# Kernel optimization log

Hardware: AMD Instinct MI355X
Metric: run time of the kernel (lower is better)

The kernel has to match this reference:

```python
import jax, jax.numpy as jnp
import numpy as np

B, N, F, D, H = 4, 2048, 128, 64, 4
NEG = -1000000000.0


def setup_inputs() -> dict:
    key = jax.random.key(0)
    k1, k2, k3, k4 = jax.random.split(key, 4)
    X = jax.random.normal(k1, (B, N, F), dtype=jnp.float32)
    A = jax.random.randint(k2, (N, N), 0, 2, dtype=jnp.int32)
    kernels = jax.random.normal(k3, (H, F, D), dtype=jnp.float32) * 0.1
    attn_kernels = jax.random.normal(k4, (H, D), dtype=jnp.float32) * 0.1
    return {"X": X, "A": A, "kernels": kernels, "attn_kernels": attn_kernels}


def reference(X, A, kernels, attn_kernels):
    # h: per-head linear projection  [H,B,N,D]
    h = jnp.einsum('bnf,hfd->hbnd', X, kernels)
    # per-node scalar scores e_i = h @ a  [H,B,N]
    s = jnp.einsum('hbnd,hd->hbn', h, attn_kernels)
    # pairwise additive score e_ij = relu(s_i + s_j)  [H,B,N,N]
    e = jax.nn.relu(s[:, :, :, None] + s[:, :, None, :])
    e = jnp.where(A[None, None, :, :] > 0, e, NEG)
    alpha = jax.nn.softmax(e, axis=-1)
    # dropout is identity at inference
    h_prime = jnp.einsum('hbnm,hbmd->hbnd', alpha, h)
    out = jnp.mean(h_prime, axis=0)           # mean over heads -> [B,N,D]
    return jax.nn.leaky_relu(out, negative_slope=0.2)
```

## Files before the change

### kernel.cpp

```cpp
#include <hip/hip_runtime.h>
#include <hip/hip_bf16.h>
#include <hip/hip_fp16.h>

typedef __attribute__((ext_vector_type(8))) short short8;
typedef __attribute__((ext_vector_type(8))) _Float16 f16x8;
typedef __attribute__((ext_vector_type(2))) _Float16 f16x2;
typedef __attribute__((ext_vector_type(4))) float f32x4;
typedef __attribute__((ext_vector_type(4))) unsigned int u32x4;
typedef unsigned short u16;
typedef unsigned int u32;

constexpr int CB = 4, CN = 2048, CF = 128, CD = 64, CH = 4;
constexpr int IT = 32;

__device__ inline u32 fmap(float f) {
    u32 b = __float_as_uint(f);
    return b ^ ((u32)(((int)b) >> 31) | 0x80000000u);
}
__device__ inline float funmap(u32 u) {
    u32 b = (u & 0x80000000u) ? (u ^ 0x80000000u) : ~u;
    return __uint_as_float(b);
}
__device__ inline u16 bf16bits(float v) {
    __hip_bfloat16 b = __float2bfloat16(v);
    return *reinterpret_cast<u16*>(&b);
}

__global__ __launch_bounds__(256) void prep_k(const int* __restrict__ A,
                                              const float* __restrict__ W,
                                              u32* __restrict__ mask,
                                              u32* __restrict__ smax_u,
                                              u16* __restrict__ WThi,
                                              u16* __restrict__ WTlo) {
    int blk = blockIdx.x, t = threadIdx.x;
    if (blk < 16384) {
        int gid = blk * 256 + t;
        if (blk == 0 && t < CH * CB) smax_u[t] = 0u;
        unsigned long long mk = __ballot(A[gid] > 0);
        if ((t & 63) == 0) {
            mask[gid >> 5] = (u32)mk;
            mask[(gid >> 5) + 1] = (u32)(mk >> 32);
        }
    } else {
        int idx = (blk - 16384) * 256 + t;
        int e = idx & 7;
        int l = (idx >> 3) & 63;
        int dt = (idx >> 9) & 3;
        int kk = (idx >> 11) & 3;
        int h = idx >> 13;
        int f = kk * 32 + (l >> 4) * 8 + e;
        int d = dt * 16 + (l & 15);
        float v = W[(h * CF + f) * CD + d];
        __hip_bfloat16 bh = __float2bfloat16(v);
        WThi[idx] = *reinterpret_cast<u16*>(&bh);
        WTlo[idx] = bf16bits(v - __bfloat162float(bh));
    }
}

__global__ __launch_bounds__(256, 2) void proj_k(const float* __restrict__ X,
                                                 const u16* __restrict__ WThi,
                                                 const u16* __restrict__ WTlo,
                                                 const float* __restrict__ AK,
                                                 u16* __restrict__ hT,
                                                 float* __restrict__ sout,
                                                 u16* __restrict__ eout,
                                                 u32* __restrict__ smax_u) {
    __shared__ float tr[4][CD][17];

    int blk = blockIdx.x;
    int ntile = blk & 127;
    int b = blk >> 7;
    int n0 = ntile * 16;
    int t = threadIdx.x;
    int w = t >> 6, l = t & 63;
    int h = w;
    int row_l = l & 15, jg = l >> 4;

    const float* xrow = X + ((size_t)b * CN + n0 + row_l) * CF + jg * 8;
    const short8* whiU = reinterpret_cast<const short8*>(WThi) + (size_t)h * 1024 + l;
    const short8* wloU = reinterpret_cast<const short8*>(WTlo) + (size_t)h * 1024 + l;

    float4 xa[4], xb[4];
#pragma unroll
    for (int kk = 0; kk < 4; ++kk) {
        xa[kk] = *reinterpret_cast<const float4*>(xrow + kk * 32);
        xb[kk] = *reinterpret_cast<const float4*>(xrow + kk * 32 + 4);
    }
    short8 bhi[4][4], blo[4][4];
#pragma unroll
    for (int kk = 0; kk < 4; ++kk)
#pragma unroll
        for (int dt = 0; dt < 4; ++dt) {
            bhi[kk][dt] = whiU[(kk * 4 + dt) * 64];
            blo[kk][dt] = wloU[(kk * 4 + dt) * 64];
        }

    f32x4 c[4];
    f32x4 zero = {0.f, 0.f, 0.f, 0.f};
#pragma unroll
    for (int dt = 0; dt < 4; ++dt) c[dt] = zero;

#pragma unroll
    for (int kk = 0; kk < 4; ++kk) {
        float xv[8] = {xa[kk].x, xa[kk].y, xa[kk].z, xa[kk].w,
                       xb[kk].x, xb[kk].y, xb[kk].z, xb[kk].w};
        short8 ahi, alo;
#pragma unroll
        for (int e = 0; e < 8; ++e) {
            __hip_bfloat16 bh = __float2bfloat16(xv[e]);
            ahi[e] = (short)*reinterpret_cast<u16*>(&bh);
            alo[e] = (short)bf16bits(xv[e] - __bfloat162float(bh));
        }
#pragma unroll
        for (int dt = 0; dt < 4; ++dt) {
            c[dt] = __builtin_amdgcn_mfma_f32_16x16x32_bf16(ahi, bhi[kk][dt], c[dt], 0, 0, 0);
            c[dt] = __builtin_amdgcn_mfma_f32_16x16x32_bf16(ahi, blo[kk][dt], c[dt], 0, 0, 0);
            c[dt] = __builtin_amdgcn_mfma_f32_16x16x32_bf16(alo, bhi[kk][dt], c[dt], 0, 0, 0);
        }
    }

    float av[4];
#pragma unroll
    for (int dt = 0; dt < 4; ++dt) av[dt] = AK[h * CD + dt * 16 + row_l];
    float sacc[4];
#pragma unroll
    for (int r = 0; r < 4; ++r)
        sacc[r] = c[0][r] * av[0] + c[1][r] * av[1] + c[2][r] * av[2] + c[3][r] * av[3];
#pragma unroll
    for (int off = 1; off <= 8; off <<= 1)
#pragma unroll
        for (int r = 0; r < 4; ++r) sacc[r] += __shfl_xor(sacc[r], off, 64);

    float mx = fmaxf(fmaxf(sacc[0], sacc[1]), fmaxf(sacc[2], sacc[3]));
    mx = fmaxf(mx, __shfl_xor(mx, 16, 64));
    mx = fmaxf(mx, __shfl_xor(mx, 32, 64));
    if (l == 0) atomicMax(&smax_u[h * CB + b], fmap(mx));

    if (row_l == 0) {
#pragma unroll
        for (int r = 0; r < 4; ++r) {
            size_t si = (size_t)(h * CB + b) * CN + n0 + jg * 4 + r;
            sout[si] = sacc[r];
            _Float16 ev = (_Float16)__expf(sacc[r]);
            eout[si] = *reinterpret_cast<u16*>(&ev);
        }
    }

#pragma unroll
    for (int dt = 0; dt < 4; ++dt)
#pragma unroll
        for (int r = 0; r < 4; ++r) tr[w][dt * 16 + row_l][jg * 4 + r] = c[dt][r];
    __syncthreads();

    f16x8* hTs = reinterpret_cast<f16x8*>(hT);
    int jc = l >> 5, d0 = l & 31;
#pragma unroll
    for (int half = 0; half < 2; ++half) {
        f16x8 pk;
#pragma unroll
        for (int e = 0; e < 8; ++e)
            pk[e] = (_Float16)tr[w][half * 32 + d0][jc * 8 + e];
        hTs[((size_t)(h * CB + b) * 256 + ntile * 2 + jc) * 64 + half * 32 + d0] = pk;
    }
}

__global__ __launch_bounds__(1024, 4) void attn_k(const u16* __restrict__ hT,
                                                  const float* __restrict__ s_ws,
                                                  const u32* __restrict__ e_ws32,
                                                  const u32* __restrict__ smax_u,
                                                  const u32* __restrict__ mask32,
                                                  float* __restrict__ out) {
    __shared__ u32 e_sl[CH][CN / 2];
    __shared__ u32 m_lds[IT][65];
    __shared__ float cbuf[CH][2][IT][68];
    __shared__ float lbuf[CH][4][IT];

    int orig = blockIdx.x;
    int xcd = orig & 7, pos = orig >> 3;
    int b = xcd >> 1;
    int it = (xcd & 1) * 32 + pos;
    int i0 = it * IT;
    int t = threadIdx.x, w = t >> 6, l = t & 63;
    int hq = w >> 2, jq = w & 3;
    int row_l = l & 15, jg = l >> 4;

    for (int idx = t; idx < CH * (CN / 2); idx += 1024) {
        int hh = idx >> 10, j = idx & 1023;
        e_sl[hh][j] = e_ws32[(size_t)(hh * CB + b) * (CN / 2) + j];
    }
    for (int idx = t; idx < IT * 64; idx += 1024) {
        int r = idx >> 6, wd = idx & 63;
        m_lds[r][wd] = mask32[(size_t)(i0 + r) * 64 + wd];
    }
    __syncthreads();

    float smax = funmap(smax_u[hq * CB + b]);
    float si0 = s_ws[(size_t)(hq * CB + b) * CN + i0 + row_l];
    float si1 = s_ws[(size_t)(hq * CB + b) * CN + i0 + 16 + row_l];
    float m0 = fmaxf(si0 + smax, 0.f), m1 = fmaxf(si1 + smax, 0.f);
    _Float16 ei0s = (_Float16)__expf(si0 - m0), ci0s = (_Float16)__expf(-m0);
    _Float16 ei1s = (_Float16)__expf(si1 - m1), ci1s = (_Float16)__expf(-m1);
    f16x2 Ei0 = {ei0s, ei0s}, Ci0 = {ci0s, ci0s};
    f16x2 Ei1 = {ei1s, ei1s}, Ci1 = {ci1s, ci1s};

    f32x4 c0[4], c1[4], cl0, cl1;
    f32x4 zero = {0.f, 0.f, 0.f, 0.f};
#pragma unroll
    for (int dt = 0; dt < 4; ++dt) { c0[dt] = zero; c1[dt] = zero; }
    cl0 = zero; cl1 = zero;

    f16x8 ones;
#pragma unroll
    for (int e = 0; e < 8; ++e) ones[e] = (_Float16)1.0f;

    const f16x8* hp = reinterpret_cast<const f16x8*>(hT) +
                      ((size_t)(hq * CB + b) * 256 + jq * 64 + jg) * 64 + row_l;

    f16x8 bfA[4], bfB[4];
#pragma unroll
    for (int dt = 0; dt < 4; ++dt) bfA[dt] = hp[dt * 16];

#define ATTN_STEP(KK, BCUR, BNXT, KNXT)                                          \
    do {                                                                         \
        _Pragma("unroll") for (int dt = 0; dt < 4; ++dt)                         \
            BNXT[dt] = hp[(KNXT) * 256 + dt * 16];                               \
        int jw = jq * 256 + (KK) * 16 + jg * 4;                                  \
        u32x4 ejw = *reinterpret_cast<const u32x4*>(&e_sl[hq][jw]);              \
        u32 by0 = m_lds[row_l][jq * 16 + (KK)] >> (jg * 8);                      \
        u32 by1 = m_lds[16 + row_l][jq * 16 + (KK)] >> (jg * 8);                 \
        u32x4 af0w, af1w;                                                        \
        _Pragma("unroll") for (int p = 0; p < 4; ++p) {                          \
            u32 ewv = ejw[p];                                                    \
            f16x2 e2 = __builtin_bit_cast(f16x2, ewv);                           \
            f16x2 t0 = __builtin_elementwise_max(Ei0 * e2, Ci0);                 \
            f16x2 t1 = __builtin_elementwise_max(Ei1 * e2, Ci1);                 \
            u32 mk0 = (((by0 >> (2 * p)) & 1u) ? 0xFFFFu : 0u) |                 \
                      (((by0 >> (2 * p + 1)) & 1u) ? 0xFFFF0000u : 0u);          \
            u32 mk1 = (((by1 >> (2 * p)) & 1u) ? 0xFFFFu : 0u) |                 \
                      (((by1 >> (2 * p + 1)) & 1u) ? 0xFFFF0000u : 0u);          \
            af0w[p] = __builtin_bit_cast(u32, t0) & mk0;                         \
            af1w[p] = __builtin_bit_cast(u32, t1) & mk1;                         \
        }                                                                        \
        f16x8 af0 = __builtin_bit_cast(f16x8, af0w);                             \
        f16x8 af1 = __builtin_bit_cast(f16x8, af1w);                             \
        __builtin_amdgcn_s_setprio(1);                                           \
        _Pragma("unroll") for (int dt = 0; dt < 4; ++dt) {                       \
            c0[dt] = __builtin_amdgcn_mfma_f32_16x16x32_f16(af0, BCUR[dt], c0[dt], 0, 0, 0); \
            c1[dt] = __builtin_amdgcn_mfma_f32_16x16x32_f16(af1, BCUR[dt], c1[dt], 0, 0, 0); \
        }                                                                        \
        cl0 = __builtin_amdgcn_mfma_f32_16x16x32_f16(af0, ones, cl0, 0, 0, 0);   \
        cl1 = __builtin_amdgcn_mfma_f32_16x16x32_f16(af1, ones, cl1, 0, 0, 0);   \
        __builtin_amdgcn_s_setprio(0);                                           \
    } while (0)

#pragma unroll 1
    for (int kp = 0; kp < 16; kp += 2) {
        ATTN_STEP(kp, bfA, bfB, kp + 1);
        int kn = (kp + 2 < 16) ? kp + 2 : 15;
        ATTN_STEP(kp + 1, bfB, bfA, kn);
    }
#undef ATTN_STEP

    int slot = jq & 1;
    if (row_l == 0)
#pragma unroll
        for (int r = 0; r < 4; ++r) {
            lbuf[hq][jq][jg * 4 + r] = cl0[r];
            lbuf[hq][jq][16 + jg * 4 + r] = cl1[r];
        }
    if (jq < 2) {
#pragma unroll
        for (int dt = 0; dt < 4; ++dt)
#pragma unroll
            for (int r = 0; r < 4; ++r) {
                cbuf[hq][slot][jg * 4 + r][dt * 16 + row_l] = c0[dt][r];
                cbuf[hq][slot][16 + jg * 4 + r][dt * 16 + row_l] = c1[dt][r];
            }
    }
    __syncthreads();
    if (jq >= 2) {
#pragma unroll
        for (int dt = 0; dt < 4; ++dt)
#pragma unroll
            for (int r = 0; r < 4; ++r) {
                cbuf[hq][slot][jg * 4 + r][dt * 16 + row_l] += c0[dt][r];
                cbuf[hq][slot][16 + jg * 4 + r][dt * 16 + row_l] += c1[dt][r];
            }
    }
    __syncthreads();

    for (int idx = t; idx < IT * CD; idx += 1024) {
        int row = idx >> 6, d = idx & 63;
        float acc = 0.f;
#pragma unroll
        for (int h = 0; h < CH; ++h) {
            float num = cbuf[h][0][row][d] + cbuf[h][1][row][d];
            float den = lbuf[h][0][row] + lbuf[h][1][row] + lbuf[h][2][row] + lbuf[h][3][row];
            acc += num / fmaxf(den, 1e-30f);
        }
        float o = acc * 0.25f;
        out[((size_t)b * CN + i0 + row) * CD + d] = o > 0.f ? o : 0.2f * o;
    }
}

extern "C" void kernel_launch(void* const* d_in, const int* in_sizes, int n_in,
                              void* d_out, int out_size, void* d_ws, size_t ws_size,
                              hipStream_t stream) {
    const float* X  = (const float*)d_in[0];
    const int*   A  = (const int*)d_in[1];
    const float* W  = (const float*)d_in[2];
    const float* AK = (const float*)d_in[3];
    float* out = (float*)d_out;

    char* wp = (char*)d_ws;
    float* s_ws = (float*)wp;    wp += 131072;
    u16* e_ws = (u16*)wp;        wp += 131072;
    u32* smax_ws = (u32*)wp;     wp += 256;
    u32* mask_ws = (u32*)wp;     wp += 524288;
    u16* hT = (u16*)wp;          wp += 4194304;
    u16* WThi = (u16*)wp;        wp += 65536;
    u16* WTlo = (u16*)wp;        wp += 65536;

    prep_k<<<16384 + 128, 256, 0, stream>>>(A, W, mask_ws, smax_ws, WThi, WTlo);
    proj_k<<<CB * (CN / 16), 256, 0, stream>>>(X, WThi, WTlo, AK, hT, s_ws, e_ws, smax_ws);
    attn_k<<<CB * (CN / IT), 1024, 0, stream>>>(hT, s_ws, (const u32*)e_ws,
                                                smax_ws, mask_ws, out);
}
```

Before: 59.40 us.

## Fuse adjacency-mask build and weight split into projection kernel

Removes the separate prep kernel. The projection kernel now builds the adjacency bitmask itself, using the h==0 blocks, and splits weights into bf16 hi/lo on the fly from a shared-memory copy of W. The projection grid is reorganised so each block handles one head and 64 rows, and smax is zeroed with a memset instead. This saves a kernel launch and the WThi/WTlo round-trip through global memory. The cost is extra per-MFMA conversion work, 32KB of LDS per block, and load imbalance, since only a quarter of the blocks do the mask work.

```diff
diff --git a/kernel.cpp b/kernel.cpp
--- a/kernel.cpp
+++ b/kernel.cpp
@@ -26,74 +26,49 @@
     return *reinterpret_cast<u16*>(&b);
 }
 
-__global__ __launch_bounds__(256) void prep_k(const int* __restrict__ A,
-                                              const float* __restrict__ W,
-                                              u32* __restrict__ mask,
-                                              u32* __restrict__ smax_u,
-                                              u16* __restrict__ WThi,
-                                              u16* __restrict__ WTlo) {
-    int blk = blockIdx.x, t = threadIdx.x;
-    if (blk < 16384) {
-        int gid = blk * 256 + t;
-        if (blk == 0 && t < CH * CB) smax_u[t] = 0u;
-        unsigned long long mk = __ballot(A[gid] > 0);
-        if ((t & 63) == 0) {
-            mask[gid >> 5] = (u32)mk;
-            mask[(gid >> 5) + 1] = (u32)(mk >> 32);
-        }
-    } else {
-        int idx = (blk - 16384) * 256 + t;
-        int e = idx & 7;
-        int l = (idx >> 3) & 63;
-        int dt = (idx >> 9) & 3;
-        int kk = (idx >> 11) & 3;
-        int h = idx >> 13;
-        int f = kk * 32 + (l >> 4) * 8 + e;
-        int d = dt * 16 + (l & 15);
-        float v = W[(h * CF + f) * CD + d];
-        __hip_bfloat16 bh = __float2bfloat16(v);
-        WThi[idx] = *reinterpret_cast<u16*>(&bh);
-        WTlo[idx] = bf16bits(v - __bfloat162float(bh));
-    }
-}
-
-__global__ __launch_bounds__(256, 2) void proj_k(const float* __restrict__ X,
-                                                 const u16* __restrict__ WThi,
-                                                 const u16* __restrict__ WTlo,
+__global__ __launch_bounds__(256, 4) void proj_k(const float* __restrict__ X,
+                                                 const int* __restrict__ A,
+                                                 const float* __restrict__ W,
                                                  const float* __restrict__ AK,
                                                  u16* __restrict__ hT,
                                                  float* __restrict__ sout,
                                                  u16* __restrict__ eout,
-                                                 u32* __restrict__ smax_u) {
+                                                 u32* __restrict__ smax_u,
+                                                 u32* __restrict__ mask_ws) {
+    __shared__ float wbuf[CF * CD];
     __shared__ float tr[4][CD][17];
 
     int blk = blockIdx.x;
-    int ntile = blk & 127;
     int b = blk >> 7;
-    int n0 = ntile * 16;
-    int t = threadIdx.x;
-    int w = t >> 6, l = t & 63;
-    int h = w;
+    int h = (blk >> 5) & 3;
+    int tile4 = blk & 31;
+    int t = threadIdx.x, w = t >> 6, l = t & 63;
     int row_l = l & 15, jg = l >> 4;
+    int n0 = tile4 * 64 + w * 16;
+
+    if (h == 0) {
+        int rowbase = tile4 * 64 + b * 16;
+        for (int iter = 0; iter < 128; ++iter) {
+            int idx = iter * 256 + t;
+            int rl2 = idx >> 11, col = idx & 2047;
+            unsigned long long mk = __ballot(A[(size_t)(rowbase + rl2) * CN + col] > 0);
+            if (l == 0) {
+                mask_ws[(rowbase + rl2) * 64 + (col >> 5)] = (u32)mk;
+                mask_ws[(rowbase + rl2) * 64 + (col >> 5) + 1] = (u32)(mk >> 32);
+            }
+        }
+    }
+
+    for (int idx = t; idx < CF * CD; idx += 256) wbuf[idx] = W[(size_t)h * CF * CD + idx];
+    __syncthreads();
 
     const float* xrow = X + ((size_t)b * CN + n0 + row_l) * CF + jg * 8;
-    const short8* whiU = reinterpret_cast<const short8*>(WThi) + (size_t)h * 1024 + l;
-    const short8* wloU = reinterpret_cast<const short8*>(WTlo) + (size_t)h * 1024 + l;
-
     float4 xa[4], xb[4];
 #pragma unroll
     for (int kk = 0; kk < 4; ++kk) {
         xa[kk] = *reinterpret_cast<const float4*>(xrow + kk * 32);
         xb[kk] = *reinterpret_cast<const float4*>(xrow + kk * 32 + 4);
     }
-    short8 bhi[4][4], blo[4][4];
-#pragma unroll
-    for (int kk = 0; kk < 4; ++kk)
-#pragma unroll
-        for (int dt = 0; dt < 4; ++dt) {
-            bhi[kk][dt] = whiU[(kk * 4 + dt) * 64];
-            blo[kk][dt] = wloU[(kk * 4 + dt) * 64];
-        }
 
     f32x4 c[4];
     f32x4 zero = {0.f, 0.f, 0.f, 0.f};
@@ -113,9 +88,17 @@
         }
 #pragma unroll
         for (int dt = 0; dt < 4; ++dt) {
-            c[dt] = __builtin_amdgcn_mfma_f32_16x16x32_bf16(ahi, bhi[kk][dt], c[dt], 0, 0, 0);
-            c[dt] = __builtin_amdgcn_mfma_f32_16x16x32_bf16(ahi, blo[kk][dt], c[dt], 0, 0, 0);
-            c[dt] = __builtin_amdgcn_mfma_f32_16x16x32_bf16(alo, bhi[kk][dt], c[dt], 0, 0, 0);
+            short8 bhi, blo;
+#pragma unroll
+            for (int e = 0; e < 8; ++e) {
+                float v = wbuf[(kk * 32 + jg * 8 + e) * CD + dt * 16 + row_l];
+                __hip_bfloat16 bh = __float2bfloat16(v);
+                bhi[e] = (short)*reinterpret_cast<u16*>(&bh);
+                blo[e] = (short)bf16bits(v - __bfloat162float(bh));
+            }
+            c[dt] = __builtin_amdgcn_mfma_f32_16x16x32_bf16(ahi, bhi, c[dt], 0, 0, 0);
+            c[dt] = __builtin_amdgcn_mfma_f32_16x16x32_bf16(ahi, blo, c[dt], 0, 0, 0);
+            c[dt] = __builtin_amdgcn_mfma_f32_16x16x32_bf16(alo, bhi, c[dt], 0, 0, 0);
         }
     }
 
@@ -153,6 +136,7 @@
     __syncthreads();
 
     f16x8* hTs = reinterpret_cast<f16x8*>(hT);
+    int ntile = tile4 * 4 + w;
     int jc = l >> 5, d0 = l & 31;
 #pragma unroll
     for (int half = 0; half < 2; ++half) {
@@ -170,7 +154,7 @@
                                                   const u32* __restrict__ smax_u,
                                                   const u32* __restrict__ mask32,
                                                   float* __restrict__ out) {
-    __shared__ u32 e_sl[CH][CN / 2];
+    __shared__ alignas(16) u32 e_sl[CH][CN / 2];
     __shared__ u32 m_lds[IT][65];
     __shared__ float cbuf[CH][2][IT][68];
     __shared__ float lbuf[CH][4][IT];
@@ -318,11 +302,10 @@
     u32* smax_ws = (u32*)wp;     wp += 256;
     u32* mask_ws = (u32*)wp;     wp += 524288;
     u16* hT = (u16*)wp;          wp += 4194304;
-    u16* WThi = (u16*)wp;        wp += 65536;
-    u16* WTlo = (u16*)wp;        wp += 65536;
-
-    prep_k<<<16384 + 128, 256, 0, stream>>>(A, W, mask_ws, smax_ws, WThi, WTlo);
-    proj_k<<<CB * (CN / 16), 256, 0, stream>>>(X, WThi, WTlo, AK, hT, s_ws, e_ws, smax_ws);
+
+    hipMemsetAsync(smax_ws, 0, 256, stream);
+    proj_k<<<CB * CH * 32, 256, 0, stream>>>(X, A, W, AK, hT, s_ws, e_ws,
+                                             smax_ws, mask_ws);
     attn_k<<<CB * (CN / IT), 1024, 0, stream>>>(hT, s_ws, (const u32*)e_ws,
                                                 smax_ws, mask_ws, out);
 }
```

After: 83.60 us. 40.7% more time.
